# Performance work log

Measured on AMD Instinct MI355X. Metric: run time of the kernel, lower is better.

The kernel has to match this reference:

```python
import jax, jax.numpy as jnp
import numpy as np

T_GRID = 2048  # static grid size (= density * data range 128)
EPS = 1e-8


def rbf(x1, x2, ls, os_):
    # x1: [B,N,1], x2: [B,M,1] -> [B,N,M]; gpytorch ScaleKernel(RBFKernel())
    d2 = (x1 - jnp.swapaxes(x2, -1, -2)) ** 2
    return os_ * jnp.exp(-0.5 * d2 / (ls * ls))


def conv1d(x, w, b):
    # x: [B,C,T], w: [O,I,5], pad 2 -> same length
    y = jax.lax.conv_general_dilated(x, w, (1,), [(2, 2)],
                                     dimension_numbers=('NCH', 'OIH', 'NCH'))
    return y + b[None, :, None]


def setup_inputs() -> dict:
    key = jax.random.key(0)
    ks = jax.random.split(key, 12)
    B, Nc, Nt = 16, 2048, 2048
    xc = jax.random.uniform(ks[0], (B, Nc, 1), jnp.float32) * 128.0
    yc = jax.random.normal(ks[1], (B, Nc, 1), jnp.float32)
    xt = jax.random.uniform(ks[2], (B, Nt, 1), jnp.float32) * 128.0
    ln2 = float(np.log(2.0))  # softplus(0), gpytorch default raw param init
    params = {
        'ls_psi': jnp.float32(ln2), 'os_psi': jnp.float32(ln2),
        'ls_rho': jnp.float32(ln2), 'os_rho': jnp.float32(ln2),
        'w1': jax.random.normal(ks[3], (16, 3, 5), jnp.float32) * 0.2,
        'b1': jnp.zeros((16,), jnp.float32),
        'w2': jax.random.normal(ks[4], (32, 16, 5), jnp.float32) * 0.1,
        'b2': jnp.zeros((32,), jnp.float32),
        'w3': jax.random.normal(ks[5], (16, 32, 5), jnp.float32) * 0.1,
        'b3': jnp.zeros((16,), jnp.float32),
        'w4': jax.random.normal(ks[6], (2, 16, 5), jnp.float32) * 0.1,
        'b4': jnp.zeros((2,), jnp.float32),
    }
    return {'xc': xc, 'yc': yc, 'xt': xt, **params}


def reference(xc, yc, xt, ls_psi, os_psi, ls_rho, os_rho,
              w1, b1, w2, b2, w3, b3, w4, b4):
    B = xc.shape[0]
    lower = jnp.minimum(xc.min(), xt.min())
    upper = jnp.maximum(xc.max(), xt.max())
    t = jnp.linspace(lower, upper, T_GRID)                      # [T]
    t = jnp.broadcast_to(t[None, :, None], (B, T_GRID, 1))      # [B,T,1]

    # SetConv encoder: h = psi(t, xc) @ phi(yc), phi = [y^0, y^1]
    Kt = rbf(t, xc, ls_psi, os_psi)                             # [B,T,Nc]
    phi = jnp.concatenate([jnp.ones_like(yc), yc], -1)          # [B,Nc,2]
    h = jnp.matmul(Kt, phi)                                     # [B,T,2]
    h0, h1 = h[..., :1], h[..., 1:]
    h1 = h1 / (h0 + EPS)
    rep = jnp.concatenate([t, h0, h1], -1).swapaxes(-1, -2)     # [B,3,T]

    # small Conv1d decoder stack
    f = jax.nn.relu(conv1d(rep, w1, b1))
    f = jax.nn.relu(conv1d(f, w2, b2))
    f = jax.nn.relu(conv1d(f, w3, b3))
    f = conv1d(f, w4, b4).swapaxes(-1, -2)                      # [B,T,2]
    f_mu, f_sigma = f[..., :1], f[..., 1:]

    # SetConv decoder onto targets
    Kr = rbf(xt, t, ls_rho, os_rho)                             # [B,Nt,T]
    mu = jnp.matmul(Kr, f_mu)                                   # [B,Nt,1]
    sigma = jnp.matmul(Kr, jax.nn.softplus(f_sigma))            # [B,Nt,1]
    return jnp.concatenate([mu, sigma], -1)                     # [B,Nt,2]
```

## Files before the change

### kernel.cpp

```cpp
#include <hip/hip_runtime.h>
#include <math.h>

#define T_GRID 2048
#define NC 2048
#define NT 2048
#define BATCH 16
#define XCUT 28.0f
#define TILE 112
#define BW 132
#define PCAP 768
#define NSB 32

__global__ __launch_bounds__(256) void k_fused(
        const float4* __restrict__ xc4, const float4* __restrict__ xt4,
        const float* __restrict__ xc, const float* __restrict__ yc,
        const float* __restrict__ ls_psi, const float* __restrict__ os_psi,
        const float* __restrict__ w1, const float* __restrict__ b1,
        const float* __restrict__ w2, const float* __restrict__ b2,
        const float* __restrict__ w3, const float* __restrict__ b3,
        const float* __restrict__ w4, const float* __restrict__ b4,
        float* __restrict__ mm, float* __restrict__ f) {
    __shared__ float rep[3][BW];
    __shared__ float L1s[16][BW];
    __shared__ __align__(16) char pool[32 * BW * 4];
    __shared__ float w1L[15][16];
    __shared__ float w2L[80][32];
    __shared__ float w3L[160][16];
    __shared__ float w4L[80][2];
    __shared__ float bL[66];

    float (*L2s)[BW] = reinterpret_cast<float (*)[BW]>(pool);
    float (*L3s)[BW] = L1s;
    float2* pts    = reinterpret_cast<float2*>(pool);
    float2* part   = reinterpret_cast<float2*>(pool + 6144);
    int*    bstart = reinterpret_cast<int*>(pool + 8192);
    int*    curi   = reinterpret_cast<int*>(pool + 8336);
    float*  bc     = reinterpret_cast<float*>(pool + 8464);

    int tid = threadIdx.x;
    int b = blockIdx.y;
    int gstart = blockIdx.x * TILE - 8;

    for (int idx = tid; idx < 240; idx += 256)  { int o = idx / 15,  r2 = idx % 15;  w1L[r2][o] = w1[idx]; }
    for (int idx = tid; idx < 2560; idx += 256) { int o = idx / 80,  r2 = idx % 80;  w2L[r2][o] = w2[idx]; }
    for (int idx = tid; idx < 2560; idx += 256) { int o = idx / 160, r2 = idx % 160; w3L[r2][o] = w3[idx]; }
    for (int idx = tid; idx < 160; idx += 256)  { int o = idx / 80,  r2 = idx % 80;  w4L[r2][o] = w4[idx]; }
    if (tid < 16) bL[tid] = b1[tid];
    if (tid < 32) bL[16 + tid] = b2[tid];
    if (tid < 16) bL[48 + tid] = b3[tid];
    if (tid < 2)  bL[64 + tid] = b4[tid];
    if (tid < 4) {
        int c = (tid < 2) ? tid : tid + 128;
        for (int r2 = 0; r2 < 3; r2++)  rep[r2][c] = 0.f;
        for (int r2 = 0; r2 < 16; r2++) L1s[r2][c] = 0.f;
    }

    float lo = 3.4e38f, hi = -3.4e38f;
    for (int i = tid; i < BATCH * NC / 4; i += 256) {
        float4 v = xc4[i];
        lo = fminf(lo, fminf(fminf(v.x, v.y), fminf(v.z, v.w)));
        hi = fmaxf(hi, fmaxf(fmaxf(v.x, v.y), fmaxf(v.z, v.w)));
    }
    for (int i = tid; i < BATCH * NT / 4; i += 256) {
        float4 v = xt4[i];
        lo = fminf(lo, fminf(fminf(v.x, v.y), fminf(v.z, v.w)));
        hi = fmaxf(hi, fmaxf(fmaxf(v.x, v.y), fmaxf(v.z, v.w)));
    }
    for (int off = 32; off; off >>= 1) {
        lo = fminf(lo, __shfl_down(lo, off));
        hi = fmaxf(hi, __shfl_down(hi, off));
    }
    if ((tid & 63) == 0) part[tid >> 6] = make_float2(lo, hi);
    __syncthreads();
    if (tid == 0) {
        for (int w = 1; w < 4; w++) {
            float2 q = part[w];
            lo = fminf(lo, q.x); hi = fmaxf(hi, q.y);
        }
        bc[0] = lo; bc[1] = hi;
        mm[0] = lo; mm[1] = hi;
    }
    __syncthreads();
    float lower = bc[0], upper = bc[1];
    float step = (upper - lower) * (1.0f / (T_GRID - 1));
    float ls = ls_psi[0], os = os_psi[0];
    float c2 = -0.72134752044f / (ls * ls);
    float R = ls * sqrtf(XCUT);

    int g0 = max(gstart, 0), g1 = min(gstart + 127, T_GRID - 1);
    float tmin = fmaf((float)g0, step, lower) - R;
    float tmax = fmaf((float)g1, step, lower) + R;
    float sbw_inv = (float)NSB / (tmax - tmin);

    if (tid < NSB + 1) bstart[tid] = 0;
    __syncthreads();
    float xv[8], yv[8];
    int bn[8];
    const float* xb = xc + b * NC;
    const float* yb = yc + b * NC;
#pragma unroll
    for (int k = 0; k < 8; k++) {
        int idx = tid + 256 * k;
        xv[k] = xb[idx];
        yv[k] = yb[idx];
        bool in = (xv[k] >= tmin) & (xv[k] <= tmax);
        bn[k] = -1;
        if (in) {
            bn[k] = min(NSB - 1, max(0, (int)((xv[k] - tmin) * sbw_inv)));
            atomicAdd(&bstart[bn[k]], 1);
        }
    }
    __syncthreads();
    if (tid == 0) {
        int run = 0;
        for (int i = 0; i < NSB; i++) { int c = bstart[i]; bstart[i] = run; run += c; }
        bstart[NSB] = run;
    }
    __syncthreads();
    if (tid < NSB) curi[tid] = bstart[tid];
    __syncthreads();
#pragma unroll
    for (int k = 0; k < 8; k++) {
        if (bn[k] >= 0) {
            int pos = atomicAdd(&curi[bn[k]], 1);
            if (pos < PCAP) pts[pos] = make_float2(xv[k], yv[k]);
        }
    }
    __syncthreads();

    {
        int p = tid & 127, rr = tid >> 7;
        int gp = gstart + p;
        bool pvalid = (gp >= 0 && gp < T_GRID);
        float t = fmaf((float)gp, step, lower);
        int s = 0, e = 0;
        if (pvalid) {
            int b0 = min(NSB - 1, max(0, (int)((t - R - tmin) * sbw_inv)));
            int b1 = min(NSB - 1, max(0, (int)((t + R - tmin) * sbw_inv)));
            s = bstart[b0];
            e = min(bstart[b1 + 1], PCAP);
        }
        float S0 = 0.f, S1 = 0.f;
        for (int j = s + rr; j < e; j += 2) {
            float2 xy = pts[j];
            float d = t - xy.x;
            float ev = exp2f(d * d * c2);
            S0 += ev;
            S1 = fmaf(ev, xy.y, S1);
        }
        __syncthreads();
        part[tid] = make_float2(S0, S1);
        __syncthreads();
        if (tid < 128) {
            float2 q = part[tid + 128];
            S0 += q.x; S1 += q.y;
            float h0 = os * S0;
            float h1 = os * S1 / (h0 + 1e-8f);
            rep[0][p + 2] = pvalid ? t : 0.f;
            rep[1][p + 2] = pvalid ? h0 : 0.f;
            rep[2][p + 2] = pvalid ? h1 : 0.f;
        }
    }
    __syncthreads();

    {
        if (tid < 4) {
            int c = (tid < 2) ? tid : tid + 128;
            for (int r2 = 0; r2 < 32; r2++) L2s[r2][c] = 0.f;
        }
        int o = tid & 15, s0 = (tid >> 4) << 3;
        float acc[8];
        float bias = bL[o];
#pragma unroll
        for (int s = 0; s < 8; s++) acc[s] = bias;
        for (int i = 0; i < 3; i++) {
            float x[12];
#pragma unroll
            for (int j = 0; j < 12; j++) x[j] = rep[i][s0 + j];
#pragma unroll
            for (int k = 0; k < 5; k++) {
                float w = w1L[i * 5 + k][o];
#pragma unroll
                for (int s = 0; s < 8; s++) acc[s] = fmaf(x[s + k], w, acc[s]);
            }
        }
        __syncthreads();
#pragma unroll
        for (int s = 0; s < 8; s++) {
            int p = s0 + s, gp = gstart + p;
            bool vv = (p >= 2 && p < 126 && gp >= 0 && gp < T_GRID);
            L1s[o][p + 2] = vv ? fmaxf(acc[s], 0.f) : 0.f;
        }
    }
    __syncthreads();

    {
        int o = tid & 31, s0 = (tid >> 5) << 4;
        float acc[16];
        float bias = bL[16 + o];
#pragma unroll
        for (int s = 0; s < 16; s++) acc[s] = bias;
        for (int i = 0; i < 16; i++) {
            float x[20];
#pragma unroll
            for (int j = 0; j < 20; j++) x[j] = L1s[i][s0 + j];
#pragma unroll
            for (int k = 0; k < 5; k++) {
                float w = w2L[i * 5 + k][o];
#pragma unroll
                for (int s = 0; s < 16; s++) acc[s] = fmaf(x[s + k], w, acc[s]);
            }
        }
#pragma unroll
        for (int s = 0; s < 16; s++) {
            int p = s0 + s, gp = gstart + p;
            bool vv = (p >= 4 && p < 124 && gp >= 0 && gp < T_GRID);
            L2s[o][p + 2] = vv ? fmaxf(acc[s], 0.f) : 0.f;
        }
    }
    __syncthreads();

    {
        int o = tid & 15, s0 = (tid >> 4) << 3;
        float acc[8];
        float bias = bL[48 + o];
#pragma unroll
        for (int s = 0; s < 8; s++) acc[s] = bias;
        for (int i = 0; i < 32; i++) {
            float x[12];
#pragma unroll
            for (int j = 0; j < 12; j++) x[j] = L2s[i][s0 + j];
#pragma unroll
            for (int k = 0; k < 5; k++) {
                float w = w3L[i * 5 + k][o];
#pragma unroll
                for (int s = 0; s < 8; s++) acc[s] = fmaf(x[s + k], w, acc[s]);
            }
        }
        __syncthreads();
#pragma unroll
        for (int s = 0; s < 8; s++) {
            int p = s0 + s, gp = gstart + p;
            bool vv = (p >= 6 && p < 122 && gp >= 0 && gp < T_GRID);
            L3s[o][p + 2] = vv ? fmaxf(acc[s], 0.f) : 0.f;
        }
    }
    __syncthreads();

    {
        int o = tid & 1, p = tid >> 1;
        float a = bL[64 + o];
        for (int i = 0; i < 16; i++) {
#pragma unroll
            for (int k = 0; k < 5; k++) {
                a = fmaf(L3s[i][p + k], w4L[i * 5 + k][o], a);
            }
        }
        int gp = gstart + p;
        if (p >= 8 && p < 120 && gp >= 0 && gp < T_GRID) {
            if (o) {
                float sp = fmaxf(a, 0.f) + log1pf(expf(-fabsf(a)));
                f[2 * (b * T_GRID + gp) + 1] = sp;
            } else {
                f[2 * (b * T_GRID + gp)] = a;
            }
        }
    }
}

__global__ __launch_bounds__(256) void k_out(const float* __restrict__ xt,
                                             const float* __restrict__ ls_rho,
                                             const float* __restrict__ os_rho,
                                             const float* __restrict__ mm,
                                             const float2* __restrict__ f,
                                             float2* __restrict__ out) {
    __shared__ float2 sf[T_GRID];
    __shared__ float2 part[256];
    int b = blockIdx.y, tid = threadIdx.x;
    int it = blockIdx.x * 64 + (tid & 63);
    int r = tid >> 6;
    float lower = mm[0], upper = mm[1];
    float step = (upper - lower) * (1.0f / (T_GRID - 1));
    float invstep = 1.0f / step;
    float ls = ls_rho[0], os = os_rho[0];
    float c2 = -0.72134752044f / (ls * ls);
    float R = ls * sqrtf(XCUT);
    float x = xt[b * NT + it];

    const float2* fb = f + b * T_GRID;
    for (int k = tid; k < T_GRID; k += 256) sf[k] = fb[k];
    __syncthreads();

    int j0 = max(0, (int)floorf((x - R - lower) * invstep));
    int j1 = min(T_GRID - 1, (int)ceilf((x + R - lower) * invstep));

    float Smu = 0.f, Ssg = 0.f;
    float jf = (float)(j0 + r);
    for (int j = j0 + r; j <= j1; j += 4) {
        float2 v = sf[j];
        float d = x - fmaf(jf, step, lower);
        float e = exp2f(d * d * c2);
        Smu = fmaf(e, v.x, Smu);
        Ssg = fmaf(e, v.y, Ssg);
        jf += 4.0f;
    }
    part[tid] = make_float2(Smu, Ssg);
    __syncthreads();
    if (r == 0) {
#pragma unroll
        for (int q = 64; q < 256; q += 64) {
            float2 pp = part[tid + q];
            Smu += pp.x; Ssg += pp.y;
        }
        out[b * NT + it] = make_float2(os * Smu, os * Ssg);
    }
}

extern "C" void kernel_launch(void* const* d_in, const int* in_sizes, int n_in,
                              void* d_out, int out_size, void* d_ws, size_t ws_size,
                              hipStream_t stream) {
    const float* xc = (const float*)d_in[0];
    const float* yc = (const float*)d_in[1];
    const float* xt = (const float*)d_in[2];
    const float* ls_psi = (const float*)d_in[3];
    const float* os_psi = (const float*)d_in[4];
    const float* ls_rho = (const float*)d_in[5];
    const float* os_rho = (const float*)d_in[6];
    const float* w1 = (const float*)d_in[7];
    const float* b1 = (const float*)d_in[8];
    const float* w2 = (const float*)d_in[9];
    const float* b2 = (const float*)d_in[10];
    const float* w3 = (const float*)d_in[11];
    const float* b3 = (const float*)d_in[12];
    const float* w4 = (const float*)d_in[13];
    const float* b4 = (const float*)d_in[14];

    char* ws = (char*)d_ws;
    float* mm = (float*)ws;
    float* f  = (float*)(ws + 64);

    int ntiles = (T_GRID + TILE - 1) / TILE;
    k_fused<<<dim3(ntiles, BATCH), dim3(256), 0, stream>>>(
        (const float4*)xc, (const float4*)xt, xc, yc, ls_psi, os_psi,
        w1, b1, w2, b2, w3, b3, w4, b4, mm, f);

    k_out<<<dim3(NT / 64, BATCH), dim3(256), 0, stream>>>(
        xt, ls_rho, os_rho, mm, (const float2*)f, (float2*)d_out);
}
```

Before: 130.2 us.

## Hoist global min/max into separate kernel and widen fused kernel to 512 threads

Moves the global min/max reduction, which every fused block used to recompute redundantly over all of xc and xt, into a single 1024-thread kernel that writes the bounds once. The fused kernel now runs 512 threads per block with the per-thread conv work halved, and the point lists are split into separate x/y shared arrays. The row stride is padded to 133 to reduce LDS bank conflicts, and a couple of barriers are removed. This adds one extra kernel launch with a serial dependency, and the single-block reduction may be latency bound.

```diff
diff --git a/kernel.cpp b/kernel.cpp
--- a/kernel.cpp
+++ b/kernel.cpp
@@ -7,19 +7,50 @@
 #define BATCH 16
 #define XCUT 28.0f
 #define TILE 112
-#define BW 132
+#define BW 133
 #define PCAP 768
 #define NSB 32
 
-__global__ __launch_bounds__(256) void k_fused(
-        const float4* __restrict__ xc4, const float4* __restrict__ xt4,
+__global__ __launch_bounds__(1024) void k_minmax(const float4* __restrict__ xc4,
+                                                 const float4* __restrict__ xt4,
+                                                 float* __restrict__ mm) {
+    float4 va[8], vb[8];
+    int tid = threadIdx.x;
+#pragma unroll
+    for (int k = 0; k < 8; k++) va[k] = xc4[tid + 1024 * k];
+#pragma unroll
+    for (int k = 0; k < 8; k++) vb[k] = xt4[tid + 1024 * k];
+    float lo = 3.4e38f, hi = -3.4e38f;
+#pragma unroll
+    for (int k = 0; k < 8; k++) {
+        lo = fminf(lo, fminf(fminf(va[k].x, va[k].y), fminf(va[k].z, va[k].w)));
+        hi = fmaxf(hi, fmaxf(fmaxf(va[k].x, va[k].y), fmaxf(va[k].z, va[k].w)));
+        lo = fminf(lo, fminf(fminf(vb[k].x, vb[k].y), fminf(vb[k].z, vb[k].w)));
+        hi = fmaxf(hi, fmaxf(fmaxf(vb[k].x, vb[k].y), fmaxf(vb[k].z, vb[k].w)));
+    }
+    for (int off = 32; off; off >>= 1) {
+        lo = fminf(lo, __shfl_down(lo, off));
+        hi = fmaxf(hi, __shfl_down(hi, off));
+    }
+    __shared__ float slo[16], shi[16];
+    int lane = tid & 63, wv = tid >> 6;
+    if (lane == 0) { slo[wv] = lo; shi[wv] = hi; }
+    __syncthreads();
+    if (tid == 0) {
+        for (int w = 1; w < 16; w++) { lo = fminf(lo, slo[w]); hi = fmaxf(hi, shi[w]); }
+        mm[0] = lo; mm[1] = hi;
+    }
+}
+
+__global__ __launch_bounds__(512) void k_fused(
         const float* __restrict__ xc, const float* __restrict__ yc,
         const float* __restrict__ ls_psi, const float* __restrict__ os_psi,
+        const float* __restrict__ mm,
         const float* __restrict__ w1, const float* __restrict__ b1,
         const float* __restrict__ w2, const float* __restrict__ b2,
         const float* __restrict__ w3, const float* __restrict__ b3,
         const float* __restrict__ w4, const float* __restrict__ b4,
-        float* __restrict__ mm, float* __restrict__ f) {
+        float* __restrict__ f) {
     __shared__ float rep[3][BW];
     __shared__ float L1s[16][BW];
     __shared__ __align__(16) char pool[32 * BW * 4];
@@ -31,20 +62,20 @@
 
     float (*L2s)[BW] = reinterpret_cast<float (*)[BW]>(pool);
     float (*L3s)[BW] = L1s;
-    float2* pts    = reinterpret_cast<float2*>(pool);
+    float*  px     = reinterpret_cast<float*>(pool);
+    float*  py     = reinterpret_cast<float*>(pool + 3072);
     float2* part   = reinterpret_cast<float2*>(pool + 6144);
-    int*    bstart = reinterpret_cast<int*>(pool + 8192);
-    int*    curi   = reinterpret_cast<int*>(pool + 8336);
-    float*  bc     = reinterpret_cast<float*>(pool + 8464);
+    int*    bstart = reinterpret_cast<int*>(pool + 10240);
+    int*    curi   = reinterpret_cast<int*>(pool + 10376);
 
     int tid = threadIdx.x;
     int b = blockIdx.y;
     int gstart = blockIdx.x * TILE - 8;
 
-    for (int idx = tid; idx < 240; idx += 256)  { int o = idx / 15,  r2 = idx % 15;  w1L[r2][o] = w1[idx]; }
-    for (int idx = tid; idx < 2560; idx += 256) { int o = idx / 80,  r2 = idx % 80;  w2L[r2][o] = w2[idx]; }
-    for (int idx = tid; idx < 2560; idx += 256) { int o = idx / 160, r2 = idx % 160; w3L[r2][o] = w3[idx]; }
-    for (int idx = tid; idx < 160; idx += 256)  { int o = idx / 80,  r2 = idx % 80;  w4L[r2][o] = w4[idx]; }
+    for (int idx = tid; idx < 240; idx += 512)  { int o = idx / 15,  r2 = idx % 15;  w1L[r2][o] = w1[idx]; }
+    for (int idx = tid; idx < 2560; idx += 512) { int o = idx / 80,  r2 = idx % 80;  w2L[r2][o] = w2[idx]; }
+    for (int idx = tid; idx < 2560; idx += 512) { int o = idx / 160, r2 = idx % 160; w3L[r2][o] = w3[idx]; }
+    for (int idx = tid; idx < 160; idx += 512)  { int o = idx / 80,  r2 = idx % 80;  w4L[r2][o] = w4[idx]; }
     if (tid < 16) bL[tid] = b1[tid];
     if (tid < 32) bL[16 + tid] = b2[tid];
     if (tid < 16) bL[48 + tid] = b3[tid];
@@ -55,33 +86,7 @@
         for (int r2 = 0; r2 < 16; r2++) L1s[r2][c] = 0.f;
     }
 
-    float lo = 3.4e38f, hi = -3.4e38f;
-    for (int i = tid; i < BATCH * NC / 4; i += 256) {
-        float4 v = xc4[i];
-        lo = fminf(lo, fminf(fminf(v.x, v.y), fminf(v.z, v.w)));
-        hi = fmaxf(hi, fmaxf(fmaxf(v.x, v.y), fmaxf(v.z, v.w)));
-    }
-    for (int i = tid; i < BATCH * NT / 4; i += 256) {
-        float4 v = xt4[i];
-        lo = fminf(lo, fminf(fminf(v.x, v.y), fminf(v.z, v.w)));
-        hi = fmaxf(hi, fmaxf(fmaxf(v.x, v.y), fmaxf(v.z, v.w)));
-    }
-    for (int off = 32; off; off >>= 1) {
-        lo = fminf(lo, __shfl_down(lo, off));
-        hi = fmaxf(hi, __shfl_down(hi, off));
-    }
-    if ((tid & 63) == 0) part[tid >> 6] = make_float2(lo, hi);
-    __syncthreads();
-    if (tid == 0) {
-        for (int w = 1; w < 4; w++) {
-            float2 q = part[w];
-            lo = fminf(lo, q.x); hi = fmaxf(hi, q.y);
-        }
-        bc[0] = lo; bc[1] = hi;
-        mm[0] = lo; mm[1] = hi;
-    }
-    __syncthreads();
-    float lower = bc[0], upper = bc[1];
+    float lower = mm[0], upper = mm[1];
     float step = (upper - lower) * (1.0f / (T_GRID - 1));
     float ls = ls_psi[0], os = os_psi[0];
     float c2 = -0.72134752044f / (ls * ls);
@@ -94,13 +99,13 @@
 
     if (tid < NSB + 1) bstart[tid] = 0;
     __syncthreads();
-    float xv[8], yv[8];
-    int bn[8];
+    float xv[4], yv[4];
+    int bn[4];
     const float* xb = xc + b * NC;
     const float* yb = yc + b * NC;
 #pragma unroll
-    for (int k = 0; k < 8; k++) {
-        int idx = tid + 256 * k;
+    for (int k = 0; k < 4; k++) {
+        int idx = tid + 512 * k;
         xv[k] = xb[idx];
         yv[k] = yb[idx];
         bool in = (xv[k] >= tmin) & (xv[k] <= tmax);
@@ -120,10 +125,10 @@
     if (tid < NSB) curi[tid] = bstart[tid];
     __syncthreads();
 #pragma unroll
-    for (int k = 0; k < 8; k++) {
+    for (int k = 0; k < 4; k++) {
         if (bn[k] >= 0) {
             int pos = atomicAdd(&curi[bn[k]], 1);
-            if (pos < PCAP) pts[pos] = make_float2(xv[k], yv[k]);
+            if (pos < PCAP) { px[pos] = xv[k]; py[pos] = yv[k]; }
         }
     }
     __syncthreads();
@@ -141,19 +146,19 @@
             e = min(bstart[b1 + 1], PCAP);
         }
         float S0 = 0.f, S1 = 0.f;
-        for (int j = s + rr; j < e; j += 2) {
-            float2 xy = pts[j];
-            float d = t - xy.x;
+        for (int j = s + rr; j < e; j += 4) {
+            float xj = px[j], yj = py[j];
+            float d = t - xj;
             float ev = exp2f(d * d * c2);
             S0 += ev;
-            S1 = fmaf(ev, xy.y, S1);
-        }
-        __syncthreads();
+            S1 = fmaf(ev, yj, S1);
+        }
         part[tid] = make_float2(S0, S1);
         __syncthreads();
         if (tid < 128) {
-            float2 q = part[tid + 128];
-            S0 += q.x; S1 += q.y;
+            float2 q1 = part[tid + 128], q2 = part[tid + 256], q3 = part[tid + 384];
+            S0 += q1.x + q2.x + q3.x;
+            S1 += q1.y + q2.y + q3.y;
             float h0 = os * S0;
             float h1 = os * S1 / (h0 + 1e-8f);
             rep[0][p + 2] = pvalid ? t : 0.f;
@@ -168,25 +173,24 @@
             int c = (tid < 2) ? tid : tid + 128;
             for (int r2 = 0; r2 < 32; r2++) L2s[r2][c] = 0.f;
         }
-        int o = tid & 15, s0 = (tid >> 4) << 3;
-        float acc[8];
+        int o = tid & 15, s0 = (tid >> 4) << 2;
+        float acc[4];
         float bias = bL[o];
 #pragma unroll
-        for (int s = 0; s < 8; s++) acc[s] = bias;
+        for (int s = 0; s < 4; s++) acc[s] = bias;
         for (int i = 0; i < 3; i++) {
-            float x[12];
-#pragma unroll
-            for (int j = 0; j < 12; j++) x[j] = rep[i][s0 + j];
+            float x[8];
+#pragma unroll
+            for (int j = 0; j < 8; j++) x[j] = rep[i][s0 + j];
 #pragma unroll
             for (int k = 0; k < 5; k++) {
                 float w = w1L[i * 5 + k][o];
 #pragma unroll
-                for (int s = 0; s < 8; s++) acc[s] = fmaf(x[s + k], w, acc[s]);
-            }
-        }
-        __syncthreads();
-#pragma unroll
-        for (int s = 0; s < 8; s++) {
+                for (int s = 0; s < 4; s++) acc[s] = fmaf(x[s + k], w, acc[s]);
+            }
+        }
+#pragma unroll
+        for (int s = 0; s < 4; s++) {
             int p = s0 + s, gp = gstart + p;
             bool vv = (p >= 2 && p < 126 && gp >= 0 && gp < T_GRID);
             L1s[o][p + 2] = vv ? fmaxf(acc[s], 0.f) : 0.f;
@@ -195,24 +199,24 @@
     __syncthreads();
 
     {
-        int o = tid & 31, s0 = (tid >> 5) << 4;
-        float acc[16];
+        int o = tid & 31, s0 = (tid >> 5) << 3;
+        float acc[8];
         float bias = bL[16 + o];
 #pragma unroll
-        for (int s = 0; s < 16; s++) acc[s] = bias;
+        for (int s = 0; s < 8; s++) acc[s] = bias;
         for (int i = 0; i < 16; i++) {
-            float x[20];
-#pragma unroll
-            for (int j = 0; j < 20; j++) x[j] = L1s[i][s0 + j];
+            float x[12];
+#pragma unroll
+            for (int j = 0; j < 12; j++) x[j] = L1s[i][s0 + j];
 #pragma unroll
             for (int k = 0; k < 5; k++) {
                 float w = w2L[i * 5 + k][o];
 #pragma unroll
-                for (int s = 0; s < 16; s++) acc[s] = fmaf(x[s + k], w, acc[s]);
-            }
-        }
-#pragma unroll
-        for (int s = 0; s < 16; s++) {
+                for (int s = 0; s < 8; s++) acc[s] = fmaf(x[s + k], w, acc[s]);
+            }
+        }
+#pragma unroll
+        for (int s = 0; s < 8; s++) {
             int p = s0 + s, gp = gstart + p;
             bool vv = (p >= 4 && p < 124 && gp >= 0 && gp < T_GRID);
             L2s[o][p + 2] = vv ? fmaxf(acc[s], 0.f) : 0.f;
@@ -221,25 +225,25 @@
     __syncthreads();
 
     {
-        int o = tid & 15, s0 = (tid >> 4) << 3;
-        float acc[8];
+        int o = tid & 15, s0 = (tid >> 4) << 2;
+        float acc[4];
         float bias = bL[48 + o];
 #pragma unroll
-        for (int s = 0; s < 8; s++) acc[s] = bias;
+        for (int s = 0; s < 4; s++) acc[s] = bias;
         for (int i = 0; i < 32; i++) {
-            float x[12];
-#pragma unroll
-            for (int j = 0; j < 12; j++) x[j] = L2s[i][s0 + j];
+            float x[8];
+#pragma unroll
+            for (int j = 0; j < 8; j++) x[j] = L2s[i][s0 + j];
 #pragma unroll
             for (int k = 0; k < 5; k++) {
                 float w = w3L[i * 5 + k][o];
 #pragma unroll
-                for (int s = 0; s < 8; s++) acc[s] = fmaf(x[s + k], w, acc[s]);
+                for (int s = 0; s < 4; s++) acc[s] = fmaf(x[s + k], w, acc[s]);
             }
         }
         __syncthreads();
 #pragma unroll
-        for (int s = 0; s < 8; s++) {
+        for (int s = 0; s < 4; s++) {
             int p = s0 + s, gp = gstart + p;
             bool vv = (p >= 6 && p < 122 && gp >= 0 && gp < T_GRID);
             L3s[o][p + 2] = vv ? fmaxf(acc[s], 0.f) : 0.f;
@@ -247,7 +251,7 @@
     }
     __syncthreads();
 
-    {
+    if (tid < 256) {
         int o = tid & 1, p = tid >> 1;
         float a = bL[64 + o];
         for (int i = 0; i < 16; i++) {
@@ -274,7 +278,8 @@
                                              const float* __restrict__ mm,
                                              const float2* __restrict__ f,
                                              float2* __restrict__ out) {
-    __shared__ float2 sf[T_GRID];
+    __shared__ float smx[T_GRID];
+    __shared__ float ssg[T_GRID];
     __shared__ float2 part[256];
     int b = blockIdx.y, tid = threadIdx.x;
     int it = blockIdx.x * 64 + (tid & 63);
@@ -288,7 +293,10 @@
     float x = xt[b * NT + it];
 
     const float2* fb = f + b * T_GRID;
-    for (int k = tid; k < T_GRID; k += 256) sf[k] = fb[k];
+    for (int k = tid; k < T_GRID; k += 256) {
+        float2 v = fb[k];
+        smx[k] = v.x; ssg[k] = v.y;
+    }
     __syncthreads();
 
     int j0 = max(0, (int)floorf((x - R - lower) * invstep));
@@ -297,11 +305,10 @@
     float Smu = 0.f, Ssg = 0.f;
     float jf = (float)(j0 + r);
     for (int j = j0 + r; j <= j1; j += 4) {
-        float2 v = sf[j];
         float d = x - fmaf(jf, step, lower);
         float e = exp2f(d * d * c2);
-        Smu = fmaf(e, v.x, Smu);
-        Ssg = fmaf(e, v.y, Ssg);
+        Smu = fmaf(e, smx[j], Smu);
+        Ssg = fmaf(e, ssg[j], Ssg);
         jf += 4.0f;
     }
     part[tid] = make_float2(Smu, Ssg);
@@ -339,10 +346,12 @@
     float* mm = (float*)ws;
     float* f  = (float*)(ws + 64);
 
+    k_minmax<<<dim3(1), dim3(1024), 0, stream>>>((const float4*)xc, (const float4*)xt, mm);
+
     int ntiles = (T_GRID + TILE - 1) / TILE;
-    k_fused<<<dim3(ntiles, BATCH), dim3(256), 0, stream>>>(
-        (const float4*)xc, (const float4*)xt, xc, yc, ls_psi, os_psi,
-        w1, b1, w2, b2, w3, b3, w4, b4, mm, f);
+    k_fused<<<dim3(ntiles, BATCH), dim3(512), 0, stream>>>(
+        xc, yc, ls_psi, os_psi, mm,
+        w1, b1, w2, b2, w3, b3, w4, b4, f);
 
     k_out<<<dim3(NT / 64, BATCH), dim3(256), 0, stream>>>(
         xt, ls_rho, os_rho, mm, (const float2*)f, (float2*)d_out);
```

Measured after the change: 113.0 us. 13.2% less time.
